# Kernel optimization log

Measured on AMD Instinct MI355X. Metric: run time of the kernel, lower is better.

## Reference

```python
import jax, jax.numpy as jnp
import numpy as np

D_MODEL = 768
D_HEAD = 64
BATCH = 2
SEQ = 4096


def setup_inputs() -> dict:
    key = jax.random.key(0)
    k1, k2, k3, k4, k5 = jax.random.split(key, 5)
    x = jax.random.normal(k1, (BATCH, SEQ, D_MODEL), dtype=jnp.float32)
    # causal mask as the module expects: (seq_len, seq_len) float, 1 where attend allowed
    mask = jnp.tril(jnp.ones((SEQ, SEQ), dtype=jnp.float32))
    # weights initialized like the module: randn / sqrt(d_model)
    scale = 1.0 / np.sqrt(D_MODEL)
    Wq = jax.random.normal(k2, (D_HEAD, D_MODEL), dtype=jnp.float32) * scale
    Wk = jax.random.normal(k3, (D_HEAD, D_MODEL), dtype=jnp.float32) * scale
    Wv = jax.random.normal(k4, (D_HEAD, D_MODEL), dtype=jnp.float32) * scale
    Wo = jax.random.normal(k5, (D_MODEL, D_HEAD), dtype=jnp.float32) * scale
    return {"x": x, "mask": mask, "Wq": Wq, "Wk": Wk, "Wv": Wv, "Wo": Wo}


def reference(x, mask, Wq, Wk, Wv, Wo):
    # q,k,v: (B, S, d_head); Linear with weight (out,in) => x @ W.T
    q = jnp.einsum('bsm,hm->bsh', x, Wq)
    k = jnp.einsum('bsm,hm->bsh', x, Wk)
    v = jnp.einsum('bsm,hm->bsh', x, Wv)
    scores = jnp.einsum('bqd,bkd->bqk', q, k) / np.sqrt(D_HEAD)  # (B,S,S)
    seq_len = x.shape[1]
    m = mask[:seq_len, :seq_len]
    # faithful to the torch code: tril(scores) - 1e10 * (1 - mask)
    scores = jnp.tril(scores) - 1e10 * (1.0 - m)
    attn = jax.nn.softmax(scores, axis=-1)
    z = jnp.einsum('bqk,bkd->bqd', attn, v)  # (B,S,d_head)
    out = jnp.einsum('bsh,mh->bsm', z, Wo)   # (B,S,d_model)
    return out
```

## Files before the change

kernel.cpp:

```cpp
#include <hip/hip_runtime.h>
#include <stdint.h>

#define SEQ 4096
#define DM 768
#define DH 64

typedef __attribute__((ext_vector_type(8))) short short8;
typedef __attribute__((ext_vector_type(4))) short short4v;
typedef __attribute__((ext_vector_type(4))) float f32x4;
typedef __attribute__((ext_vector_type(2))) uint32_t uint2v;

#define LOG2E 1.4426950408889634f

static __device__ __forceinline__ short bf16r(float f) {
  union { float f; uint32_t u; } v; v.f = f;
  uint32_t u = v.u;
  return (short)((u + 0x7FFFu + ((u >> 16) & 1u)) >> 16);
}

static __device__ __forceinline__ float bf16f(uint16_t u) {
  union { uint32_t u; float f; } v; v.u = ((uint32_t)u) << 16;
  return v.f;
}

static __device__ __forceinline__ uint32_t cvtpk(float a, float b) {
  uint32_t r;
  asm("v_cvt_pk_bf16_f32 %0, %1, %2" : "=v"(r) : "v"(a), "v"(b));
  return r;
}

static __device__ __forceinline__ int swz(int row, int b) {
  return row * 128 + (b ^ ((row & 7) << 4));
}

static __device__ __forceinline__ void glds16(const void* g, void* l) {
  __builtin_amdgcn_global_load_lds(
      (const __attribute__((address_space(1))) uint32_t*)g,
      (__attribute__((address_space(3))) uint32_t*)l, 16, 0, 0);
}

__global__ __launch_bounds__(256) void convert_w(
    const float* __restrict__ Wq, const float* __restrict__ Wk,
    const float* __restrict__ Wv, const float* __restrict__ Wo,
    uint16_t* __restrict__ Wbp, uint16_t* __restrict__ Wob) {
  int id = blockIdx.x * 256 + threadIdx.x;
  if (id < 18432) {
    int nh = id / 9216, rem = id % 9216;
    int t = rem / 768, rem2 = rem % 768;
    int r = rem2 >> 3, g = rem2 & 7;
    int row = nh * 96 + r;
    const float* src = (row < 64) ? (Wq + (size_t)row * DM)
                     : (row < 128) ? (Wk + (size_t)(row - 64) * DM)
                                   : (Wv + (size_t)(row - 128) * DM);
    const float sc = (row < 64) ? (0.125f * LOG2E) : 1.0f;
    float4 v0 = *(const float4*)(src + t * 64 + g * 8);
    float4 v1 = *(const float4*)(src + t * 64 + g * 8 + 4);
    union { uint32_t u[4]; short8 s; } pk;
    pk.u[0] = cvtpk(v0.x * sc, v0.y * sc);
    pk.u[1] = cvtpk(v0.z * sc, v0.w * sc);
    pk.u[2] = cvtpk(v1.x * sc, v1.y * sc);
    pk.u[3] = cvtpk(v1.z * sc, v1.w * sc);
    char* dst = (char*)Wbp + (size_t)nh * 147456 + t * 12288 + swz(r, g * 16);
    *(short8*)dst = pk.s;
  } else if (id < 30720) {
    int tt = id - 18432;
    int row = tt >> 4, c4 = tt & 15;
    float4 v = *(const float4*)(Wo + (size_t)row * DH + c4 * 4);
    short4v pk = { bf16r(v.x), bf16r(v.y), bf16r(v.z), bf16r(v.w) };
    *(short4v*)(Wob + (size_t)row * DH + c4 * 4) = pk;
  }
}

__global__ __launch_bounds__(256) void qkv_proj(
    const float* __restrict__ x, const uint16_t* __restrict__ Wbp,
    uint16_t* __restrict__ qg, uint16_t* __restrict__ kg, uint16_t* __restrict__ vg) {
  __shared__ char smem[49152] __attribute__((aligned(16)));
  const int tid = threadIdx.x;
  const int lane = tid & 63, wv = tid >> 6;
  const int l15 = lane & 15, l4 = lane >> 4;
  const int row0 = blockIdx.x * 32;
  const int nh = blockIdx.y;
  const char* wsrc = (const char*)Wbp + (size_t)nh * 147456;

  const int xr = tid >> 4, xc4 = tid & 15;
  const int mh = wv & 1, ng = wv >> 1;

  const float* xp0 = x + (size_t)(row0 + xr) * DM + xc4 * 4;
  const float* xp1 = x + (size_t)(row0 + 16 + xr) * DM + xc4 * 4;

  f32x4 acc[3];
  #pragma unroll
  for (int j = 0; j < 3; ++j) acc[j] = (f32x4){0.f, 0.f, 0.f, 0.f};

  float4 xrg[2][2];
  xrg[0][0] = *(const float4*)(xp0);
  xrg[0][1] = *(const float4*)(xp1);
  #pragma unroll
  for (int i = 0; i < 3; ++i)
    glds16(wsrc + i * 1024 + wv * 3072 + lane * 16,
           smem + 12288 + wv * 3072 + i * 1024);
  __builtin_amdgcn_sched_barrier(0);
  xrg[1][0] = *(const float4*)(xp0 + 64);
  xrg[1][1] = *(const float4*)(xp1 + 64);
  #pragma unroll
  for (int i = 0; i < 3; ++i)
    glds16(wsrc + 12288 + wv * 3072 + i * 1024 + lane * 16,
           smem + 12288 + 12288 + wv * 3072 + i * 1024);
  __builtin_amdgcn_sched_barrier(0);
  {
    uint2v p0 = { cvtpk(xrg[0][0].x, xrg[0][0].y), cvtpk(xrg[0][0].z, xrg[0][0].w) };
    *(uint2v*)(smem + swz(xr, xc4 * 8)) = p0;
    uint2v p1 = { cvtpk(xrg[0][1].x, xrg[0][1].y), cvtpk(xrg[0][1].z, xrg[0][1].w) };
    *(uint2v*)(smem + swz(xr + 16, xc4 * 8)) = p1;
  }

  #pragma unroll
  for (int t = 0; t < 12; ++t) {
    asm volatile("s_waitcnt lgkmcnt(0)" ::: "memory");
    if (t < 11) {
      asm volatile("s_waitcnt vmcnt(5)" ::: "memory");
    } else {
      asm volatile("s_waitcnt vmcnt(0)" ::: "memory");
    }
    __builtin_amdgcn_s_barrier();
    if (t < 10) {
      const int k2 = (t + 2) * 64;
      xrg[t & 1][0] = *(const float4*)(xp0 + k2);
      xrg[t & 1][1] = *(const float4*)(xp1 + k2);
      #pragma unroll
      for (int i = 0; i < 3; ++i)
        glds16(wsrc + (t + 2) * 12288 + wv * 3072 + i * 1024 + lane * 16,
               smem + 12288 + ((t + 2) % 3) * 12288 + wv * 3072 + i * 1024);
      __builtin_amdgcn_sched_barrier(0);
    }
    {
      char* Xl = smem + (t % 3) * 4096;
      char* Wl = smem + 12288 + (t % 3) * 12288;
      #pragma unroll
      for (int kc = 0; kc < 2; ++kc) {
        short8 af = *(const short8*)(Xl + swz(mh * 16 + l15, kc * 64 + l4 * 16));
        #pragma unroll
        for (int j = 0; j < 3; ++j) {
          int tl = ng * 3 + j;
          short8 bfv = *(const short8*)(Wl + swz(tl * 16 + l15, kc * 64 + l4 * 16));
          acc[j] = __builtin_amdgcn_mfma_f32_16x16x32_bf16(af, bfv, acc[j], 0, 0, 0);
        }
      }
    }
    if (t < 11) {
      char* Xn = smem + ((t + 1) % 3) * 4096;
      float4 a0 = xrg[(t + 1) & 1][0], a1 = xrg[(t + 1) & 1][1];
      uint2v p0 = { cvtpk(a0.x, a0.y), cvtpk(a0.z, a0.w) };
      *(uint2v*)(Xn + swz(xr, xc4 * 8)) = p0;
      uint2v p1 = { cvtpk(a1.x, a1.y), cvtpk(a1.z, a1.w) };
      *(uint2v*)(Xn + swz(xr + 16, xc4 * 8)) = p1;
    }
  }
  #pragma unroll
  for (int j = 0; j < 3; ++j) {
    int NT = nh * 6 + ng * 3 + j;
    uint16_t* dst = (NT < 4) ? qg : (NT < 8) ? kg : vg;
    int cb = (NT & 3) * 16 + l15;
    #pragma unroll
    for (int r = 0; r < 4; ++r) {
      int row = row0 + mh * 16 + l4 * 4 + r;
      dst[(size_t)row * DH + cb] = (uint16_t)bf16r(acc[j][r]);
    }
  }
}

__global__ __launch_bounds__(256) void attn_split(
    const uint16_t* __restrict__ qg, const uint16_t* __restrict__ kg,
    const uint16_t* __restrict__ vg, uint16_t* __restrict__ zg,
    uint16_t* __restrict__ Opart, float* __restrict__ Ml, int CHUNK, int MAXCH) {
  __shared__ char smem[32768 + 4 * 2048] __attribute__((aligned(16)));

  const int tid = threadIdx.x;
  const int lane = tid & 63, wv = tid >> 6;
  const int l15 = lane & 15, l4 = lane >> 4;
  const int qt = blockIdx.x, ch = blockIdx.y, b = blockIdx.z;
  const int q0 = qt << 6;
  const int kv_lim = q0 + 64;
  const int kv_begin = ch * CHUNK;
  if (kv_begin >= kv_lim) return;
  const int kv_end = min(kv_begin + CHUNK, kv_lim);
  const int ntiles = (kv_end - kv_begin) >> 6;

  const uint16_t* qb = qg + (size_t)b * SEQ * DH;
  const uint16_t* kb = kg + (size_t)b * SEQ * DH;
  const uint16_t* vb = vg + (size_t)b * SEQ * DH;

  const int qrow = q0 + wv * 16 + l15;
  short8 qf0 = *(const short8*)(qb + (size_t)qrow * DH + l4 * 8);
  short8 qf1 = *(const short8*)(qb + (size_t)qrow * DH + 32 + l4 * 8);

  int koffA[4], koffB[4], voffA[4], voffB[4];
  #pragma unroll
  for (int n = 0; n < 4; ++n) {
    koffA[n] = swz(n * 16 + l15, l4 * 16);
    koffB[n] = swz(n * 16 + l15, 64 + l4 * 16);
    int dr = n * 16 + l15;
    voffA[n] = 8192 + dr * 128 + ((l4 * 16) ^ ((dr & 7) << 4));
    voffB[n] = 8192 + dr * 128 + ((64 + l4 * 16) ^ ((dr & 7) << 4));
  }
  int pwoff[4];
  #pragma unroll
  for (int n = 0; n < 4; ++n) pwoff[n] = 32768 + wv * 2048 + swz(l15, n * 32 + l4 * 8);
  const int proff0 = 32768 + wv * 2048 + swz(l15, l4 * 16);
  const int proff1 = 32768 + wv * 2048 + swz(l15, 64 + l4 * 16);

  const int ku = tid - 128;
  const int vg_ = tid >> 3, vdg = tid & 7;
  short8 sreg[4];
  int soff[8];
  if (tid >= 128) {
    #pragma unroll
    for (int i = 0; i < 4; ++i) {
      int c = ku + (i << 7);
      soff[i] = swz(c >> 3, (c & 7) * 16);
    }
  } else {
    #pragma unroll
    for (int j = 0; j < 8; ++j) {
      int d = vdg * 8 + j;
      soff[j] = 8192 + d * 128 + ((vg_ * 8) ^ ((d & 7) << 4));
    }
  }

#define LOAD_REGS(KV0)                                                              \
  if (tid >= 128) {                                                                 \
    _Pragma("unroll")                                                               \
    for (int i = 0; i < 4; ++i) {                                                   \
      int c = ku + (i << 7);                                                        \
      sreg[i] = *(const short8*)(kb + (size_t)((KV0) + (c >> 3)) * DH + (c & 7) * 8); \
    }                                                                               \
  } else {                                                                          \
    _Pragma("unroll")                                                               \
    for (int i = 0; i < 4; ++i)                                                     \
      sreg[i] = *(const short8*)(vb + (size_t)((KV0) + vg_ * 4 + i) * DH + vdg * 8); \
  }

#define STAGE_WRITE(BUF)                                                            \
  {                                                                                 \
    char* base_ = smem + ((BUF) << 14);                                             \
    if (tid >= 128) {                                                               \
      _Pragma("unroll")                                                             \
      for (int i = 0; i < 4; ++i) *(short8*)(base_ + soff[i]) = sreg[i];            \
    } else {                                                                        \
      _Pragma("unroll")                                                             \
      for (int j = 0; j < 8; ++j) {                                                 \
        short4v pk = { sreg[0][j], sreg[1][j], sreg[2][j], sreg[3][j] };            \
        *(short4v*)(base_ + soff[j]) = pk;                                          \
      }                                                                             \
    }                                                                               \
  }

  LOAD_REGS(kv_begin);
  STAGE_WRITE(0);

  f32x4 oaccT[4];
  #pragma unroll
  for (int n = 0; n < 4; ++n) oaccT[n] = (f32x4){0.f, 0.f, 0.f, 0.f};
  float lrun = 0.f;

  for (int T = 0; T < ntiles; ++T) {
    const int kv0 = kv_begin + (T << 6);
    const bool more = (T + 1 < ntiles);
    if (more) { LOAD_REGS(kv0 + 64); }
    __syncthreads();
    char* cb_ = smem + ((T & 1) << 14);

    f32x4 sacc[4];
    #pragma unroll
    for (int n = 0; n < 4; ++n) sacc[n] = (f32x4){0.f, 0.f, 0.f, 0.f};
    __builtin_amdgcn_s_setprio(1);
    #pragma unroll
    for (int n = 0; n < 4; ++n) {
      short8 kf0 = *(const short8*)(cb_ + koffA[n]);
      sacc[n] = __builtin_amdgcn_mfma_f32_16x16x32_bf16(kf0, qf0, sacc[n], 0, 0, 0);
      short8 kf1 = *(const short8*)(cb_ + koffB[n]);
      sacc[n] = __builtin_amdgcn_mfma_f32_16x16x32_bf16(kf1, qf1, sacc[n], 0, 0, 0);
    }
    __builtin_amdgcn_s_setprio(0);

    if (more) { STAGE_WRITE((T + 1) & 1); }

    if (kv0 + 63 > q0) {
      #pragma unroll
      for (int n = 0; n < 4; ++n) {
        #pragma unroll
        for (int r = 0; r < 4; ++r) {
          int kvg = kv0 + n * 16 + l4 * 4 + r;
          if (kvg > qrow) sacc[n][r] = -1e30f;
        }
      }
    }

    float ls = 0.f;
    #pragma unroll
    for (int n = 0; n < 4; ++n) {
      #pragma unroll
      for (int r = 0; r < 4; ++r) {
        float p = __builtin_amdgcn_exp2f(sacc[n][r]);
        sacc[n][r] = p;
        ls += p;
      }
    }
    ls += __shfl_xor(ls, 16);
    ls += __shfl_xor(ls, 32);
    lrun += ls;

    #pragma unroll
    for (int n = 0; n < 4; ++n) {
      uint2v pk = { cvtpk(sacc[n][0], sacc[n][1]), cvtpk(sacc[n][2], sacc[n][3]) };
      *(uint2v*)(smem + pwoff[n]) = pk;
    }
    asm volatile("s_waitcnt lgkmcnt(0)" ::: "memory");
    short8 pa0 = *(const short8*)(smem + proff0);
    short8 pa1 = *(const short8*)(smem + proff1);
    __builtin_amdgcn_s_setprio(1);
    #pragma unroll
    for (int n = 0; n < 4; ++n) {
      short8 vf0 = *(const short8*)(cb_ + voffA[n]);
      oaccT[n] = __builtin_amdgcn_mfma_f32_16x16x32_bf16(vf0, pa0, oaccT[n], 0, 0, 0);
      short8 vf1 = *(const short8*)(cb_ + voffB[n]);
      oaccT[n] = __builtin_amdgcn_mfma_f32_16x16x32_bf16(vf1, pa1, oaccT[n], 0, 0, 0);
    }
    __builtin_amdgcn_s_setprio(0);
  }
#undef LOAD_REGS
#undef STAGE_WRITE

  const int rl = wv * 16 + l15;
  if (MAXCH == 1) {
    float invl = 1.0f / lrun;
    uint16_t* zb = zg + (size_t)b * SEQ * DH;
    #pragma unroll
    for (int n = 0; n < 4; ++n) {
      short4v pk = { bf16r(oaccT[n][0] * invl), bf16r(oaccT[n][1] * invl),
                     bf16r(oaccT[n][2] * invl), bf16r(oaccT[n][3] * invl) };
      *(short4v*)(zb + (size_t)(q0 + rl) * DH + n * 16 + l4 * 4) = pk;
    }
  } else {
    const size_t slot = ((size_t)(b << 6) + qt) * MAXCH + ch;
    uint16_t* op = Opart + slot * 4096;
    #pragma unroll
    for (int n = 0; n < 4; ++n) {
      short4v pk = { bf16r(oaccT[n][0]), bf16r(oaccT[n][1]),
                     bf16r(oaccT[n][2]), bf16r(oaccT[n][3]) };
      *(short4v*)(op + (size_t)rl * 64 + n * 16 + l4 * 4) = pk;
    }
    if (l4 == 0) Ml[slot * 64 + rl] = lrun;
  }
}

__global__ __launch_bounds__(256) void out_proj(
    const uint16_t* __restrict__ Opart, const float* __restrict__ Ml,
    const uint16_t* __restrict__ zg, const uint16_t* __restrict__ Wob,
    float* __restrict__ out, int CHUNK, int MAXCH) {
  __shared__ char smem[4096 + 32768] __attribute__((aligned(16)));
  char* Zl = smem;
  char* Wl = smem + 4096;
  const int tid = threadIdx.x;
  const int lane = tid & 63, wv = tid >> 6;
  const int l15 = lane & 15, l4 = lane >> 4;
  const int row0 = blockIdx.x * 32;
  const int col0 = blockIdx.y * 256;

  {
    const int r = tid >> 3, c0 = (tid & 7) << 3;
    if (MAXCH == 1) {
      short8 v = *(const short8*)(zg + (size_t)(row0 + r) * DH + c0);
      *(short8*)(Zl + swz(r, c0 * 2)) = v;
    } else {
      const int b = row0 >> 12;
      const int rlb = row0 & 4095;
      const int qt = rlb >> 6, q0 = qt << 6;
      const int row_local = (rlb & 63) + r;
      const int nch = (q0 + 64 + CHUNK - 1) / CHUNK;
      const size_t sbase = ((size_t)(b << 6) + qt) * MAXCH;
      float a[8] = {0.f, 0.f, 0.f, 0.f, 0.f, 0.f, 0.f, 0.f};
      float wsum = 0.f;
      for (int ch = 0; ch < nch; ++ch) {
        const size_t s = sbase + ch;
        wsum += Ml[s * 64 + row_local];
        short8 v = *(const short8*)(Opart + s * 4096 + (size_t)row_local * 64 + c0);
        #pragma unroll
        for (int j = 0; j < 8; ++j) a[j] += bf16f((uint16_t)v[j]);
      }
      float inv = 1.0f / wsum;
      short8 pk;
      #pragma unroll
      for (int j = 0; j < 8; ++j) pk[j] = bf16r(a[j] * inv);
      *(short8*)(Zl + swz(r, c0 * 2)) = pk;
    }
  }
  #pragma unroll
  for (int i = 0; i < 8; ++i) {
    int id = tid + (i << 8);
    int m = id >> 3, c8 = id & 7;
    short8 vw = *(const short8*)(Wob + (size_t)(col0 + m) * DH + c8 * 8);
    *(short8*)(Wl + swz(m, c8 * 16)) = vw;
  }
  __syncthreads();

  const int mh = wv & 1, ng = wv >> 1;
  short8 af0 = *(const short8*)(Zl + swz(mh * 16 + l15, l4 * 16));
  short8 af1 = *(const short8*)(Zl + swz(mh * 16 + l15, 64 + l4 * 16));
  f32x4 acc[8];
  #pragma unroll
  for (int j = 0; j < 8; ++j) acc[j] = (f32x4){0.f, 0.f, 0.f, 0.f};
  #pragma unroll
  for (int j = 0; j < 8; ++j) {
    int nt = ng * 8 + j;
    short8 b0 = *(const short8*)(Wl + swz(nt * 16 + l15, l4 * 16));
    acc[j] = __builtin_amdgcn_mfma_f32_16x16x32_bf16(af0, b0, acc[j], 0, 0, 0);
    short8 b1 = *(const short8*)(Wl + swz(nt * 16 + l15, 64 + l4 * 16));
    acc[j] = __builtin_amdgcn_mfma_f32_16x16x32_bf16(af1, b1, acc[j], 0, 0, 0);
  }
  #pragma unroll
  for (int j = 0; j < 8; ++j) {
    int nt = ng * 8 + j;
    #pragma unroll
    for (int r = 0; r < 4; ++r) {
      int row = row0 + mh * 16 + l4 * 4 + r;
      int col = col0 + nt * 16 + l15;
      out[(size_t)row * DM + col] = acc[j][r];
    }
  }
}

extern "C" void kernel_launch(void* const* d_in, const int* in_sizes, int n_in,
                              void* d_out, int out_size, void* d_ws, size_t ws_size,
                              hipStream_t stream) {
  const float* x  = (const float*)d_in[0];
  const float* Wq = (const float*)d_in[2];
  const float* Wk = (const float*)d_in[3];
  const float* Wv = (const float*)d_in[4];
  const float* Wo = (const float*)d_in[5];
  float* out = (float*)d_out;

  const size_t N = (size_t)2 * SEQ * DH;
  uint16_t* qg = (uint16_t*)d_ws;
  uint16_t* kg = qg + N;
  uint16_t* vg = kg + N;
  uint16_t* zg = vg + N;
  uint16_t* Wbp = zg + N;
  const size_t WBE = (size_t)192 * DM;
  uint16_t* Wob = Wbp + WBE;
  const size_t WOE = (size_t)DM * DH;
  uint16_t* Opart = Wob + WOE;

  int maxch = 16;
  while (maxch > 1) {
    size_t slots = (size_t)2 * 64 * maxch;
    size_t need = 4 * N * 2 + WBE * 2 + WOE * 2 + slots * (4096 * 2 + 64 * 4);
    if (need <= ws_size) break;
    maxch >>= 1;
  }
  const int CHUNK = SEQ / maxch;
  float* Ml = (float*)(Opart + (size_t)2 * 64 * maxch * 4096);

  convert_w<<<120, 256, 0, stream>>>(Wq, Wk, Wv, Wo, Wbp, Wob);
  qkv_proj<<<dim3(256, 2), 256, 0, stream>>>(x, Wbp, qg, kg, vg);
  attn_split<<<dim3(64, maxch, 2), 256, 0, stream>>>(qg, kg, vg, zg, Opart, Ml,
                                                     CHUNK, maxch);
  out_proj<<<dim3(256, 3), 256, 0, stream>>>(Opart, Ml, zg, Wob, out, CHUNK, maxch);
}
```

Measured before the change: 47.73 us.

## Redistribute P via ds_bpermute and restage V transpose with wider LDS writes

Replaces the per-wave LDS round-trip used to reshape the softmax probabilities into the MFMA A-operand layout with cross-lane ds_bpermute shuffles plus selects, removing the 8KB P scratch area and the lgkmcnt wait. It also changes how V tiles are loaded and transposed into LDS: each thread reads 8 rows of 4 columns and writes 16-byte transposed chunks instead of 8-byte ones. This lowers LDS footprint and store count, but adds 16 bpermute ops per tile and more narrow global loads for V.

```diff
diff --git a/kernel.cpp b/kernel.cpp
--- a/kernel.cpp
+++ b/kernel.cpp
@@ -173,7 +173,7 @@
     const uint16_t* __restrict__ qg, const uint16_t* __restrict__ kg,
     const uint16_t* __restrict__ vg, uint16_t* __restrict__ zg,
     uint16_t* __restrict__ Opart, float* __restrict__ Ml, int CHUNK, int MAXCH) {
-  __shared__ char smem[32768 + 4 * 2048] __attribute__((aligned(16)));
+  __shared__ char smem[32768] __attribute__((aligned(16)));
 
   const int tid = threadIdx.x;
   const int lane = tid & 63, wv = tid >> 6;
@@ -203,16 +203,12 @@
     voffA[n] = 8192 + dr * 128 + ((l4 * 16) ^ ((dr & 7) << 4));
     voffB[n] = 8192 + dr * 128 + ((64 + l4 * 16) ^ ((dr & 7) << 4));
   }
-  int pwoff[4];
-  #pragma unroll
-  for (int n = 0; n < 4; ++n) pwoff[n] = 32768 + wv * 2048 + swz(l15, n * 32 + l4 * 8);
-  const int proff0 = 32768 + wv * 2048 + swz(l15, l4 * 16);
-  const int proff1 = 32768 + wv * 2048 + swz(l15, 64 + l4 * 16);
 
   const int ku = tid - 128;
-  const int vg_ = tid >> 3, vdg = tid & 7;
+  const int kvgV = tid >> 4, dqV = tid & 15;
   short8 sreg[4];
-  int soff[8];
+  short4v vr8[8];
+  int soff[4], vwoff[4];
   if (tid >= 128) {
     #pragma unroll
     for (int i = 0; i < 4; ++i) {
@@ -221,38 +217,38 @@
     }
   } else {
     #pragma unroll
-    for (int j = 0; j < 8; ++j) {
-      int d = vdg * 8 + j;
-      soff[j] = 8192 + d * 128 + ((vg_ * 8) ^ ((d & 7) << 4));
-    }
-  }
-
-#define LOAD_REGS(KV0)                                                              \
-  if (tid >= 128) {                                                                 \
-    _Pragma("unroll")                                                               \
-    for (int i = 0; i < 4; ++i) {                                                   \
-      int c = ku + (i << 7);                                                        \
-      sreg[i] = *(const short8*)(kb + (size_t)((KV0) + (c >> 3)) * DH + (c & 7) * 8); \
-    }                                                                               \
-  } else {                                                                          \
-    _Pragma("unroll")                                                               \
-    for (int i = 0; i < 4; ++i)                                                     \
-      sreg[i] = *(const short8*)(vb + (size_t)((KV0) + vg_ * 4 + i) * DH + vdg * 8); \
-  }
-
-#define STAGE_WRITE(BUF)                                                            \
-  {                                                                                 \
-    char* base_ = smem + ((BUF) << 14);                                             \
-    if (tid >= 128) {                                                               \
-      _Pragma("unroll")                                                             \
-      for (int i = 0; i < 4; ++i) *(short8*)(base_ + soff[i]) = sreg[i];            \
-    } else {                                                                        \
-      _Pragma("unroll")                                                             \
-      for (int j = 0; j < 8; ++j) {                                                 \
-        short4v pk = { sreg[0][j], sreg[1][j], sreg[2][j], sreg[3][j] };            \
-        *(short4v*)(base_ + soff[j]) = pk;                                          \
-      }                                                                             \
-    }                                                                               \
+    for (int c = 0; c < 4; ++c)
+      vwoff[c] = 8192 + swz(dqV * 4 + c, kvgV * 16);
+  }
+
+#define LOAD_REGS(KV0)                                                               \
+  if (tid >= 128) {                                                                  \
+    _Pragma("unroll")                                                                \
+    for (int i = 0; i < 4; ++i) {                                                    \
+      int c = ku + (i << 7);                                                         \
+      sreg[i] = *(const short8*)(kb + (size_t)((KV0) + (c >> 3)) * DH + (c & 7) * 8);  \
+    }                                                                                \
+  } else {                                                                           \
+    _Pragma("unroll")                                                                \
+    for (int i = 0; i < 8; ++i)                                                      \
+      vr8[i] = *(const short4v*)(vb + (size_t)((KV0) + kvgV * 8 + i) * DH + dqV * 4);  \
+  }
+
+#define STAGE_WRITE(BUF)                                                             \
+  {                                                                                  \
+    char* base_ = smem + ((BUF) << 14);                                              \
+    if (tid >= 128) {                                                                \
+      _Pragma("unroll")                                                              \
+      for (int i = 0; i < 4; ++i) *(short8*)(base_ + soff[i]) = sreg[i];             \
+    } else {                                                                         \
+      _Pragma("unroll")                                                              \
+      for (int c = 0; c < 4; ++c) {                                                  \
+        short8 w;                                                                    \
+        _Pragma("unroll")                                                            \
+        for (int i = 0; i < 8; ++i) w[i] = vr8[i][c];                                \
+        *(short8*)(base_ + vwoff[c]) = w;                                            \
+      }                                                                              \
+    }                                                                                \
   }
 
   LOAD_REGS(kv_begin);
@@ -262,6 +258,10 @@
   #pragma unroll
   for (int n = 0; n < 4; ++n) oaccT[n] = (f32x4){0.f, 0.f, 0.f, 0.f};
   float lrun = 0.f;
+
+  const int bp0 = (((l4 & 1) << 5) + l15) << 2;
+  const int bp1 = bp0 + 64;
+  const bool hi2 = (l4 >> 1) != 0;
 
   for (int T = 0; T < ntiles; ++T) {
     const int kv0 = kv_begin + (T << 6);
@@ -290,8 +290,8 @@
       for (int n = 0; n < 4; ++n) {
         #pragma unroll
         for (int r = 0; r < 4; ++r) {
-          int kvg = kv0 + n * 16 + l4 * 4 + r;
-          if (kvg > qrow) sacc[n][r] = -1e30f;
+          int kvg_ = kv0 + n * 16 + l4 * 4 + r;
+          if (kvg_ > qrow) sacc[n][r] = -1e30f;
         }
       }
     }
@@ -310,21 +310,46 @@
     ls += __shfl_xor(ls, 32);
     lrun += ls;
 
-    #pragma unroll
-    for (int n = 0; n < 4; ++n) {
-      uint2v pk = { cvtpk(sacc[n][0], sacc[n][1]), cvtpk(sacc[n][2], sacc[n][3]) };
-      *(uint2v*)(smem + pwoff[n]) = pk;
-    }
-    asm volatile("s_waitcnt lgkmcnt(0)" ::: "memory");
-    short8 pa0 = *(const short8*)(smem + proff0);
-    short8 pa1 = *(const short8*)(smem + proff1);
+    uint32_t pk[8];
+    #pragma unroll
+    for (int n = 0; n < 4; ++n) {
+      pk[n * 2]     = cvtpk(sacc[n][0], sacc[n][1]);
+      pk[n * 2 + 1] = cvtpk(sacc[n][2], sacc[n][3]);
+    }
+    union { uint32_t d[4]; short8 s; } pa0u, pa1u;
+    {
+      uint32_t x0 = __builtin_amdgcn_ds_bpermute(bp0, (int)pk[0]);
+      uint32_t x2 = __builtin_amdgcn_ds_bpermute(bp0, (int)pk[2]);
+      pa0u.d[0] = hi2 ? x2 : x0;
+      uint32_t y1 = __builtin_amdgcn_ds_bpermute(bp0, (int)pk[1]);
+      uint32_t y3 = __builtin_amdgcn_ds_bpermute(bp0, (int)pk[3]);
+      pa0u.d[1] = hi2 ? y3 : y1;
+      uint32_t z0 = __builtin_amdgcn_ds_bpermute(bp1, (int)pk[0]);
+      uint32_t z2 = __builtin_amdgcn_ds_bpermute(bp1, (int)pk[2]);
+      pa0u.d[2] = hi2 ? z2 : z0;
+      uint32_t w1 = __builtin_amdgcn_ds_bpermute(bp1, (int)pk[1]);
+      uint32_t w3 = __builtin_amdgcn_ds_bpermute(bp1, (int)pk[3]);
+      pa0u.d[3] = hi2 ? w3 : w1;
+      uint32_t x4 = __builtin_amdgcn_ds_bpermute(bp0, (int)pk[4]);
+      uint32_t x6 = __builtin_amdgcn_ds_bpermute(bp0, (int)pk[6]);
+      pa1u.d[0] = hi2 ? x6 : x4;
+      uint32_t y5 = __builtin_amdgcn_ds_bpermute(bp0, (int)pk[5]);
+      uint32_t y7 = __builtin_amdgcn_ds_bpermute(bp0, (int)pk[7]);
+      pa1u.d[1] = hi2 ? y7 : y5;
+      uint32_t z4 = __builtin_amdgcn_ds_bpermute(bp1, (int)pk[4]);
+      uint32_t z6 = __builtin_amdgcn_ds_bpermute(bp1, (int)pk[6]);
+      pa1u.d[2] = hi2 ? z6 : z4;
+      uint32_t w5 = __builtin_amdgcn_ds_bpermute(bp1, (int)pk[5]);
+      uint32_t w7 = __builtin_amdgcn_ds_bpermute(bp1, (int)pk[7]);
+      pa1u.d[3] = hi2 ? w7 : w5;
+    }
     __builtin_amdgcn_s_setprio(1);
     #pragma unroll
     for (int n = 0; n < 4; ++n) {
       short8 vf0 = *(const short8*)(cb_ + voffA[n]);
-      oaccT[n] = __builtin_amdgcn_mfma_f32_16x16x32_bf16(vf0, pa0, oaccT[n], 0, 0, 0);
+      oaccT[n] = __builtin_amdgcn_mfma_f32_16x16x32_bf16(vf0, pa0u.s, oaccT[n], 0, 0, 0);
       short8 vf1 = *(const short8*)(cb_ + voffB[n]);
-      oaccT[n] = __builtin_amdgcn_mfma_f32_16x16x32_bf16(vf1, pa1, oaccT[n], 0, 0, 0);
+      oaccT[n] = __builtin_amdgcn_mfma_f32_16x16x32_bf16(vf1, pa1u.s, oaccT[n], 0, 0, 0);
     }
     __builtin_amdgcn_s_setprio(0);
   }
@@ -337,18 +362,18 @@
     uint16_t* zb = zg + (size_t)b * SEQ * DH;
     #pragma unroll
     for (int n = 0; n < 4; ++n) {
-      short4v pk = { bf16r(oaccT[n][0] * invl), bf16r(oaccT[n][1] * invl),
-                     bf16r(oaccT[n][2] * invl), bf16r(oaccT[n][3] * invl) };
-      *(short4v*)(zb + (size_t)(q0 + rl) * DH + n * 16 + l4 * 4) = pk;
+      short4v pkv = { bf16r(oaccT[n][0] * invl), bf16r(oaccT[n][1] * invl),
+                      bf16r(oaccT[n][2] * invl), bf16r(oaccT[n][3] * invl) };
+      *(short4v*)(zb + (size_t)(q0 + rl) * DH + n * 16 + l4 * 4) = pkv;
     }
   } else {
     const size_t slot = ((size_t)(b << 6) + qt) * MAXCH + ch;
     uint16_t* op = Opart + slot * 4096;
     #pragma unroll
     for (int n = 0; n < 4; ++n) {
-      short4v pk = { bf16r(oaccT[n][0]), bf16r(oaccT[n][1]),
-                     bf16r(oaccT[n][2]), bf16r(oaccT[n][3]) };
-      *(short4v*)(op + (size_t)rl * 64 + n * 16 + l4 * 4) = pk;
+      short4v pkv = { bf16r(oaccT[n][0]), bf16r(oaccT[n][1]),
+                      bf16r(oaccT[n][2]), bf16r(oaccT[n][3]) };
+      *(short4v*)(op + (size_t)rl * 64 + n * 16 + l4 * 4) = pkv;
     }
     if (l4 == 0) Ml[slot * 64 + rl] = lrun;
   }
```

New measurement: 48.10 us. About the same (+0.8%).
